# Kernel optimization log

Hardware: AMD Instinct MI355X
Metric: run time of the kernel (lower is better)

The kernel has to match this reference:

```python
import jax, jax.numpy as jnp
import numpy as np

B, S, H, T, N = 32, 512, 1024, 8, 16


def setup_inputs() -> dict:
    key = jax.random.key(0)
    ks = jax.random.split(key, 16)
    sc = 1.0 / np.sqrt(H)
    f32 = jnp.float32
    return {
        "hidden": jax.random.normal(ks[0], (S, B, H), f32),
        "num_encoder_outputs": jax.random.normal(ks[1], (B, N, H), f32),
        "problem_q": jax.random.normal(ks[2], (B, H), f32),
        # GenerateXQs K/V projections
        "Wk": jax.random.normal(ks[3], (H, H), f32) * sc,
        "bk": jax.random.normal(ks[4], (H,), f32) * sc,
        "Wv": jax.random.normal(ks[5], (H, H), f32) * sc,
        "bv": jax.random.normal(ks[6], (H,), f32) * sc,
        # XToQ K/V projections
        "Wk2": jax.random.normal(ks[7], (H, H), f32) * sc,
        "bk2": jax.random.normal(ks[8], (H,), f32) * sc,
        "Wv2": jax.random.normal(ks[9], (H, H), f32) * sc,
        "bv2": jax.random.normal(ks[10], (H,), f32) * sc,
        # XToQ single-layer LSTM (PyTorch gate order i,f,g,o)
        "W_ih": jax.random.normal(ks[11], (4 * H, H), f32) * sc,
        "W_hh": jax.random.normal(ks[12], (4 * H, H), f32) * sc,
        "b_ih": jax.random.normal(ks[13], (4 * H,), f32) * sc,
        "b_hh": jax.random.normal(ks[14], (4 * H,), f32) * sc,
        "num_xs": T,  # all batch items generate T tokens (required for torch.stack)
    }


def _attend(x_bh, keys_bsh, values_bsh):
    # softmax(x @ K^T) @ V, batched over b
    scores = jnp.einsum("bh,bsh->bs", x_bh, keys_bsh)
    attn = jax.nn.softmax(scores, axis=-1)
    return jnp.einsum("bs,bsh->bh", attn, values_bsh)


def reference(hidden, num_encoder_outputs, problem_q,
              Wk, bk, Wv, bv, Wk2, bk2, Wv2, bv2,
              W_ih, W_hh, b_ih, b_hh, num_xs):
    Tn = int(num_xs)
    hidden2 = jnp.swapaxes(hidden, 0, 1)           # [B,S,H]
    keys = hidden2 @ Wk.T + bk                      # [B,S,H]
    values = hidden2 @ Wv.T + bv                    # [B,S,H]

    def gen_step(x, _):
        xn = _attend(x, keys, values)
        return xn, xn

    if Tn > 1:
        _, rest = jax.lax.scan(gen_step, problem_q, None, length=Tn - 1)  # [T-1,B,H]
        final_xs = jnp.concatenate(
            [problem_q[:, None, :], jnp.swapaxes(rest, 0, 1)], axis=1)    # [B,T,H]
    else:
        final_xs = problem_q[:, None, :]

    # XToQ: parallel attention of each generated x over the (projected) hidden
    keys2 = hidden2 @ Wk2.T + bk2
    values2 = hidden2 @ Wv2.T + bv2
    scores = jnp.einsum("bth,bsh->bts", final_xs, keys2)
    attn = jax.nn.softmax(scores, axis=-1)
    qs = jnp.einsum("bts,bsh->bth", attn, values2)  # [B,T,H]

    if Tn > 1:
        # single-layer LSTM over time (PyTorch gate order: i, f, g, o)
        def lstm_step(carry, x_t):
            h, c = carry
            gates = x_t @ W_ih.T + b_ih + h @ W_hh.T + b_hh  # [B,4H]
            i, f, g, o = jnp.split(gates, 4, axis=-1)
            i, f, o = jax.nn.sigmoid(i), jax.nn.sigmoid(f), jax.nn.sigmoid(o)
            g = jnp.tanh(g)
            c = f * c + i * g
            h = o * jnp.tanh(c)
            return (h, c), h

        h0 = jnp.zeros((qs.shape[0], H), qs.dtype)
        c0 = jnp.zeros((qs.shape[0], H), qs.dtype)
        _, outs = jax.lax.scan(lstm_step, (h0, c0), jnp.swapaxes(qs, 0, 1))  # [T,B,H]
        # original appends out1[0] (the t=0 LSTM output) as an extra token
        final_qs = jnp.concatenate([qs, outs[0][:, None, :]], axis=1)        # [B,T+1,H]
    else:
        final_qs = qs

    updated_hidden = jnp.swapaxes(jnp.concatenate([hidden2, final_xs], axis=1), 0, 1)  # [S+T,B,H]
    updated_nums = jnp.concatenate([num_encoder_outputs, final_xs], axis=1)             # [B,N+T,H]
    return (final_qs, updated_hidden, updated_nums)
```

## Files before the change

kernel.cpp:

```cpp
#include <hip/hip_runtime.h>
#include <math.h>

#define Bn 32
#define Sn 512
#define Hn 1024
#define Tn 8
#define Nn 16
#define Gn 4096

__device__ __forceinline__ float wsum(float v){
#pragma unroll
  for (int off = 32; off; off >>= 1) v += __shfl_xor(v, off);
  return v;
}

__device__ __forceinline__ float dot16(float4 a0, float4 a1, float4 a2, float4 a3,
                                       float4 v0, float4 v1, float4 v2, float4 v3){
  float d = a0.x*v0.x + a0.y*v0.y + a0.z*v0.z + a0.w*v0.w;
  d += a1.x*v1.x + a1.y*v1.y + a1.z*v1.z + a1.w*v1.w;
  d += a2.x*v2.x + a2.y*v2.y + a2.z*v2.z + a2.w*v2.w;
  d += a3.x*v3.x + a3.y*v3.y + a3.z*v3.z + a3.w*v3.w;
  return d;
}


__global__ __launch_bounds__(256) void transpose2(
    const float* __restrict__ Wk, const float* __restrict__ Wk2,
    float* __restrict__ WkT, float* __restrict__ Wk2T){
  __shared__ float tile[32][33];
  const float* in  = blockIdx.z ? Wk2  : Wk;
  float*       outp= blockIdx.z ? Wk2T : WkT;
  int tx = threadIdx.x & 31, ty = threadIdx.x >> 5;
  int c0 = blockIdx.x * 32, r0 = blockIdx.y * 32;
#pragma unroll
  for (int k = 0; k < 4; ++k)
    tile[ty + 8*k][tx] = in[(size_t)(r0 + ty + 8*k) * Hn + c0 + tx];
  __syncthreads();
#pragma unroll
  for (int k = 0; k < 4; ++k)
    outp[(size_t)(c0 + ty + 8*k) * Hn + r0 + tx] = tile[tx][ty + 8*k];
}

__global__ __launch_bounds__(256) void prep(
    const float4* __restrict__ nums, const float4* __restrict__ pq,
    float4* __restrict__ un, float4* __restrict__ xs){
  int n = blockIdx.x, b = blockIdx.y;
  if (n < Nn) un[((size_t)b*(Nn+Tn) + n)*256 + threadIdx.x] = nums[((size_t)b*Nn + n)*256 + threadIdx.x];
  else        xs[((size_t)b*Tn)*256 + threadIdx.x] = pq[(size_t)b*256 + threadIdx.x];
}

__global__ __launch_bounds__(256) void finalize_xs(const float4* __restrict__ xs, float4* __restrict__ uh, float4* __restrict__ un){
  int t = blockIdx.x, b = blockIdx.y;
  float4 v = xs[((size_t)b*Tn + t)*256 + threadIdx.x];
  uh[(((size_t)(Sn + t))*Bn + b)*256 + threadIdx.x] = v;
  un[((size_t)b*(Nn+Tn) + Nn + t)*256 + threadIdx.x] = v;
}

template<int FIRST>
__global__ __launch_bounds__(512, 8) void attend8(
    const float* __restrict__ hidden, const float* __restrict__ xk,
    float* __restrict__ ctxp, float* __restrict__ mlp, float* __restrict__ uh)
{
  const int b = blockIdx.y, p = blockIdx.x;
  const int tid = threadIdx.x, lane = tid & 63, w = tid >> 6;
  __shared__ float sM[8], sL[8];
  __shared__ float sacc[8*1024];

  const float4* xp = (const float4*)(xk + (size_t)b*Hn) + lane;
  float4 q0 = xp[0], q1 = xp[64], q2 = xp[128], q3 = xp[192];

  const int s0 = p*16 + w*2;
  size_t r0 = ((size_t)(s0+0)*Bn + b)*Hn, r1 = ((size_t)(s0+1)*Bn + b)*Hn;
  const float4* rp0 = (const float4*)(hidden + r0) + lane;
  const float4* rp1 = (const float4*)(hidden + r1) + lane;
  float4 u0=rp0[0], u1=rp0[64], u2=rp0[128], u3=rp0[192];
  float4 v0=rp1[0], v1=rp1[64], v2=rp1[128], v3=rp1[192];
  if (FIRST){
    float4* w0p = (float4*)(uh + r0) + lane;
    float4* w1p = (float4*)(uh + r1) + lane;
    w0p[0]=u0; w0p[64]=u1; w0p[128]=u2; w0p[192]=u3;
    w1p[0]=v0; w1p[64]=v1; w1p[128]=v2; w1p[192]=v3;
  }
  float d0 = dot16(q0,q1,q2,q3, u0,u1,u2,u3);
  float d1 = dot16(q0,q1,q2,q3, v0,v1,v2,v3);
#pragma unroll
  for (int off = 32; off; off >>= 1){ d0 += __shfl_xor(d0, off); d1 += __shfl_xor(d1, off); }
  float m_run = fmaxf(d0, d1);
  float w0 = __expf(d0 - m_run), w1 = __expf(d1 - m_run);
  float l_run = w0 + w1;
  float4 a0 = make_float4(w0*u0.x + w1*v0.x, w0*u0.y + w1*v0.y, w0*u0.z + w1*v0.z, w0*u0.w + w1*v0.w);
  float4 a1 = make_float4(w0*u1.x + w1*v1.x, w0*u1.y + w1*v1.y, w0*u1.z + w1*v1.z, w0*u1.w + w1*v1.w);
  float4 a2 = make_float4(w0*u2.x + w1*v2.x, w0*u2.y + w1*v2.y, w0*u2.z + w1*v2.z, w0*u2.w + w1*v2.w);
  float4 a3 = make_float4(w0*u3.x + w1*v3.x, w0*u3.y + w1*v3.y, w0*u3.z + w1*v3.z, w0*u3.w + w1*v3.w);

  {
    int sl0 = (lane*4 + 0) ^ (lane & 7);
    int sl1 = (lane*4 + 1) ^ (lane & 7);
    int sl2 = (lane*4 + 2) ^ (lane & 7);
    int sl3 = (lane*4 + 3) ^ (lane & 7);
    *(float4*)(sacc + w*1024 + sl0*4) = a0;
    *(float4*)(sacc + w*1024 + sl1*4) = a1;
    *(float4*)(sacc + w*1024 + sl2*4) = a2;
    *(float4*)(sacc + w*1024 + sl3*4) = a3;
  }
  if (lane == 0){ sM[w] = m_run; sL[w] = l_run; }
  __syncthreads();
  float M = sM[0];
#pragma unroll
  for (int i = 1; i < 8; ++i) M = fmaxf(M, sM[i]);
  float wex[8];
#pragma unroll
  for (int i = 0; i < 8; ++i) wex[i] = __expf(sM[i] - M);
#pragma unroll
  for (int h0 = 0; h0 < 1024; h0 += 512){
    int c = h0 + tid;
    int k = c >> 8, l = (c >> 2) & 63, j = c & 3;
    int fo = ((((l << 2) + k) ^ (l & 7)) << 2) + j;
    float s = 0.f;
#pragma unroll
    for (int i = 0; i < 8; ++i) s = fmaf(sacc[i*1024 + fo], wex[i], s);
    ctxp[((size_t)b*32 + p)*1024 + c] = s;
  }
  if (tid == 0){
    float L = 0.f;
#pragma unroll
    for (int i = 0; i < 8; ++i) L = fmaf(sL[i], wex[i], L);
    mlp[((size_t)b*32 + p)*2]     = M;
    mlp[((size_t)b*32 + p)*2 + 1] = L;
  }
}

__global__ __launch_bounds__(256) void mv1(
    const float* __restrict__ X, int xstride,
    const float* __restrict__ M, float* __restrict__ part,
    int nj, int ktiles)
{
  __shared__ float wt[64*128];
  __shared__ float xl[64*32];
  const int t  = threadIdx.x;
  const int j0 = blockIdx.x * 128;
  const int kb = blockIdx.y;
  const int r0 = blockIdx.z * 32;
  const int R  = gridDim.z * 32;
  const int tj = t & 31, tr = t >> 5;
  float acc[4][4] = {{0.f,0.f,0.f,0.f},{0.f,0.f,0.f,0.f},{0.f,0.f,0.f,0.f},{0.f,0.f,0.f,0.f}};

  for (int kt = 0; kt < ktiles; ++kt){
    const int k0 = (kb*ktiles + kt)*64;
    __syncthreads();
    {
      int j = t >> 1;
      int kqb = (t & 1) * 8;
      const float* Mrow = M + (size_t)(j0 + j)*1024 + k0;
#pragma unroll
      for (int c = 0; c < 8; ++c){
        float4 v = *(const float4*)(Mrow + (kqb + c)*4);
        int kk = (kqb + c)*4;
        wt[(kk+0)*128 + j] = v.x;
        wt[(kk+1)*128 + j] = v.y;
        wt[(kk+2)*128 + j] = v.z;
        wt[(kk+3)*128 + j] = v.w;
      }
      int r = t >> 3;
      int kq0 = t & 7;
#pragma unroll
      for (int c = 0; c < 2; ++c){
        int kk = (kq0 + c*8)*4;
        float4 v = *(const float4*)(X + (size_t)(r0 + r)*xstride + k0 + kk);
        xl[(kk+0)*32 + r] = v.x;
        xl[(kk+1)*32 + r] = v.y;
        xl[(kk+2)*32 + r] = v.z;
        xl[(kk+3)*32 + r] = v.w;
      }
    }
    __syncthreads();
#pragma unroll 4
    for (int k = 0; k < 64; ++k){
      float4 w4 = *(const float4*)(wt + k*128 + tj*4);
      float4 x4 = *(const float4*)(xl + k*32  + tr*4);
      acc[0][0] = fmaf(x4.x, w4.x, acc[0][0]);
      acc[0][1] = fmaf(x4.x, w4.y, acc[0][1]);
      acc[0][2] = fmaf(x4.x, w4.z, acc[0][2]);
      acc[0][3] = fmaf(x4.x, w4.w, acc[0][3]);
      acc[1][0] = fmaf(x4.y, w4.x, acc[1][0]);
      acc[1][1] = fmaf(x4.y, w4.y, acc[1][1]);
      acc[1][2] = fmaf(x4.y, w4.z, acc[1][2]);
      acc[1][3] = fmaf(x4.y, w4.w, acc[1][3]);
      acc[2][0] = fmaf(x4.z, w4.x, acc[2][0]);
      acc[2][1] = fmaf(x4.z, w4.y, acc[2][1]);
      acc[2][2] = fmaf(x4.z, w4.z, acc[2][2]);
      acc[2][3] = fmaf(x4.z, w4.w, acc[2][3]);
      acc[3][0] = fmaf(x4.w, w4.x, acc[3][0]);
      acc[3][1] = fmaf(x4.w, w4.y, acc[3][1]);
      acc[3][2] = fmaf(x4.w, w4.z, acc[3][2]);
      acc[3][3] = fmaf(x4.w, w4.w, acc[3][3]);
    }
  }
  const size_t base = ((size_t)kb*R + r0 + tr*4)*nj + j0 + tj*4;
#pragma unroll
  for (int i = 0; i < 4; ++i)
    *(float4*)(part + base + (size_t)i*nj) = make_float4(acc[i][0], acc[i][1], acc[i][2], acc[i][3]);
}

__global__ __launch_bounds__(256) void mv2(
    const float* __restrict__ part, int R, int njshift, int KB,
    const float* __restrict__ b1, const float* __restrict__ b2,
    float* __restrict__ out, int rpgshift, int opg)
{
  int idx = blockIdx.x*256 + threadIdx.x;
  int nj = 1 << njshift;
  int r = idx >> njshift, j = idx & (nj - 1);
  float s = 0.f;
  if (b1) s += b1[j];
  if (b2) s += b2[j];
  size_t stride = (size_t)R << njshift;
  for (int kb = 0; kb < KB; ++kb) s += part[(size_t)kb*stride + idx];
  int orow = ((r >> rpgshift) * opg) + (r & ((1 << rpgshift) - 1));
  out[((size_t)orow << njshift) + j] = s;
}

__global__ __launch_bounds__(256) void genstep(
    const float* __restrict__ ctxp, const float* __restrict__ mlp,
    const float* __restrict__ Wv, float* __restrict__ part)
{
  __shared__ float wt[64*128];
  __shared__ float xl[64*32];
  const int t  = threadIdx.x;
  const int j0 = blockIdx.x * 128;
  const int kb = blockIdx.y;
  const int k0 = kb*64;
  const int tj = t & 31, tr = t >> 5;

  {
    int j = t >> 1;
    int kqb = (t & 1) * 8;
    const float* Mrow = Wv + (size_t)(j0 + j)*1024 + k0;
#pragma unroll
    for (int c = 0; c < 8; ++c){
      float4 v = *(const float4*)(Mrow + (kqb + c)*4);
      int kk = (kqb + c)*4;
      wt[(kk+0)*128 + j] = v.x;
      wt[(kk+1)*128 + j] = v.y;
      wt[(kk+2)*128 + j] = v.z;
      wt[(kk+3)*128 + j] = v.w;
    }
  }
  {
    int b = t >> 3, kk = (t & 7)*8;
    float mx = -1e30f;
#pragma unroll
    for (int i = 0; i < 32; ++i) mx = fmaxf(mx, mlp[((size_t)b*32 + i)*2]);
    float L = 0.f;
    float a8[8] = {0.f,0.f,0.f,0.f,0.f,0.f,0.f,0.f};
#pragma unroll 4
    for (int i = 0; i < 32; ++i){
      float m = mlp[((size_t)b*32 + i)*2];
      float l = mlp[((size_t)b*32 + i)*2 + 1];
      float we = __expf(m - mx);
      L = fmaf(l, we, L);
      const float* cp = ctxp + ((size_t)b*32 + i)*1024 + k0 + kk;
      float4 u0 = *(const float4*)cp;
      float4 u1 = *(const float4*)(cp + 4);
      a8[0] = fmaf(we, u0.x, a8[0]); a8[1] = fmaf(we, u0.y, a8[1]);
      a8[2] = fmaf(we, u0.z, a8[2]); a8[3] = fmaf(we, u0.w, a8[3]);
      a8[4] = fmaf(we, u1.x, a8[4]); a8[5] = fmaf(we, u1.y, a8[5]);
      a8[6] = fmaf(we, u1.z, a8[6]); a8[7] = fmaf(we, u1.w, a8[7]);
    }
    float inv = 1.f / L;
#pragma unroll
    for (int q = 0; q < 8; ++q) xl[(kk + q)*32 + b] = a8[q]*inv;
  }
  __syncthreads();
  float acc[4][4] = {{0.f,0.f,0.f,0.f},{0.f,0.f,0.f,0.f},{0.f,0.f,0.f,0.f},{0.f,0.f,0.f,0.f}};
#pragma unroll 4
  for (int k = 0; k < 64; ++k){
    float4 w4 = *(const float4*)(wt + k*128 + tj*4);
    float4 x4 = *(const float4*)(xl + k*32  + tr*4);
    acc[0][0] = fmaf(x4.x, w4.x, acc[0][0]);
    acc[0][1] = fmaf(x4.x, w4.y, acc[0][1]);
    acc[0][2] = fmaf(x4.x, w4.z, acc[0][2]);
    acc[0][3] = fmaf(x4.x, w4.w, acc[0][3]);
    acc[1][0] = fmaf(x4.y, w4.x, acc[1][0]);
    acc[1][1] = fmaf(x4.y, w4.y, acc[1][1]);
    acc[1][2] = fmaf(x4.y, w4.z, acc[1][2]);
    acc[1][3] = fmaf(x4.y, w4.w, acc[1][3]);
    acc[2][0] = fmaf(x4.z, w4.x, acc[2][0]);
    acc[2][1] = fmaf(x4.z, w4.y, acc[2][1]);
    acc[2][2] = fmaf(x4.z, w4.z, acc[2][2]);
    acc[2][3] = fmaf(x4.z, w4.w, acc[2][3]);
    acc[3][0] = fmaf(x4.w, w4.x, acc[3][0]);
    acc[3][1] = fmaf(x4.w, w4.y, acc[3][1]);
    acc[3][2] = fmaf(x4.w, w4.z, acc[3][2]);
    acc[3][3] = fmaf(x4.w, w4.w, acc[3][3]);
  }
  const size_t base = ((size_t)kb*32 + tr*4)*1024 + j0 + tj*4;
#pragma unroll
  for (int i = 0; i < 4; ++i)
    *(float4*)(part + base + (size_t)i*1024) = make_float4(acc[i][0], acc[i][1], acc[i][2], acc[i][3]);
}


__global__ __launch_bounds__(512) void scores2_kernel(
    const float* __restrict__ hidden, const float* __restrict__ xk2, float* __restrict__ sc)
{
  int b = blockIdx.y, p = blockIdx.x;
  int lane = threadIdx.x & 63, w = threadIdx.x >> 6;
  int t0 = (w & 3) * 2, rh = w >> 2;
  const float4* qa = (const float4*)(xk2 + ((size_t)b*Tn + t0  )*Hn) + lane;
  const float4* qb = (const float4*)(xk2 + ((size_t)b*Tn + t0+1)*Hn) + lane;
  float4 a0=qa[0], a1=qa[64], a2=qa[128], a3=qa[192];
  float4 c0=qb[0], c1=qb[64], c2=qb[128], c3=qb[192];
#pragma unroll 2
  for (int r = 0; r < 8; ++r){
    int s = p*16 + rh*8 + r;
    const float4* row = (const float4*)(hidden + ((size_t)s*Bn + b)*Hn) + lane;
    float4 v0=row[0], v1=row[64], v2=row[128], v3=row[192];
    float d0 = wsum(dot16(a0,a1,a2,a3, v0,v1,v2,v3));
    float d1 = wsum(dot16(c0,c1,c2,c3, v0,v1,v2,v3));
    if (lane == 0){
      sc[((size_t)b*Tn + t0  )*Sn + s] = d0;
      sc[((size_t)b*Tn + t0+1)*Sn + s] = d1;
    }
  }
}

__global__ __launch_bounds__(512) void ctx2f(
    const float* __restrict__ hidden, const float* __restrict__ scraw, float* __restrict__ ctx2)
{
  int b = blockIdx.y, hc = blockIdx.x, tid = threadIdx.x;
  __shared__ float al[Tn*Sn];
  for (int i = tid; i < Tn*Sn; i += 512) al[i] = scraw[(size_t)b*Tn*Sn + i];
  __syncthreads();
  {
    int r = tid >> 6, lane = tid & 63;
    float mx = -1e30f;
#pragma unroll
    for (int k = 0; k < 8; ++k) mx = fmaxf(mx, al[r*Sn + lane + k*64]);
#pragma unroll
    for (int off = 32; off; off >>= 1) mx = fmaxf(mx, __shfl_xor(mx, off));
    float e[8], s = 0.f;
#pragma unroll
    for (int k = 0; k < 8; ++k){ e[k] = __expf(al[r*Sn + lane + k*64] - mx); s += e[k]; }
#pragma unroll
    for (int off = 32; off; off >>= 1) s += __shfl_xor(s, off);
    float inv = 1.f / s;
#pragma unroll
    for (int k = 0; k < 8; ++k) al[r*Sn + lane + k*64] = e[k] * inv;
  }
  __syncthreads();
  int hloc = tid & 127, tg = tid >> 7;
  int h = hc*128 + hloc;
  int t0 = tg*2;
  float acc0 = 0.f, acc1 = 0.f;
#pragma unroll 4
  for (int s = 0; s < Sn; ++s){
    float v = hidden[((size_t)s*Bn + b)*Hn + h];
    acc0 = fmaf(al[t0*Sn + s],     v, acc0);
    acc1 = fmaf(al[(t0+1)*Sn + s], v, acc1);
  }
  ctx2[((size_t)b*Tn + t0  )*Hn + h] = acc0;
  ctx2[((size_t)b*Tn + t0+1)*Hn + h] = acc1;
}

__global__ __launch_bounds__(256) void lstm_fused(
    const float* __restrict__ part, const float* __restrict__ b_ih,
    const float* __restrict__ b_hh, float* __restrict__ fq)
{
  int idx = blockIdx.x*256 + threadIdx.x;
  int b = idx >> 10, h = idx & 1023;
  const size_t stride = (size_t)32*Gn;
  float gi = b_ih[h] + b_hh[h];
  float gg = b_ih[2048+h] + b_hh[2048+h];
  float go = b_ih[3072+h] + b_hh[3072+h];
  for (int kb = 0; kb < 16; ++kb){
    const float* pp = part + (size_t)kb*stride + (size_t)b*Gn;
    gi += pp[h]; gg += pp[2048+h]; go += pp[3072+h];
  }
  float si = 1.f/(1.f + __expf(-gi));
  float so = 1.f/(1.f + __expf(-go));
  float c  = si * tanhf(gg);
  fq[((size_t)b*(Tn+1) + Tn)*Hn + h] = so * tanhf(c);
}


extern "C" void kernel_launch(void* const* d_in, const int* in_sizes, int n_in,
                              void* d_out, int out_size, void* d_ws, size_t ws_size,
                              hipStream_t stream) {
  const float* hidden = (const float*)d_in[0];
  const float* nums   = (const float*)d_in[1];
  const float* pq     = (const float*)d_in[2];
  const float* Wk     = (const float*)d_in[3];
  const float* Wv     = (const float*)d_in[5];
  const float* bv     = (const float*)d_in[6];
  const float* Wk2    = (const float*)d_in[7];
  const float* Wv2    = (const float*)d_in[9];
  const float* bv2    = (const float*)d_in[10];
  const float* W_ih   = (const float*)d_in[11];
  const float* b_ih   = (const float*)d_in[13];
  const float* b_hh   = (const float*)d_in[14];

  float* out = (float*)d_out;
  float* fq  = out;
  float* uh  = out + (size_t)Bn*(Tn+1)*Hn;
  float* un  = uh + (size_t)(Sn+Tn)*Bn*Hn;

  float* ws    = (float*)d_ws;
  float* xs    = ws;
  float* ctxp  = ws + 262144;
  float* mlp   = ws + 1310720;
  float* xk    = ws + 1312768;
  float* xk2   = ws + 1345536;
  float* sc2   = ws + 1607680;
  float* ctx2v = ws + 1738752;
  float* partX = ws + 2000896;
  float* partK = ws + 2525184;
  float* WkT   = ws + 3049472;
  float* Wk2T  = ws + 4098048;
  float* partS = partX;
  float* partL = WkT;

  transpose2<<<dim3(32,32,2), 256, 0, stream>>>(Wk, Wk2, WkT, Wk2T);
  prep<<<dim3(Nn+1, Bn), 256, 0, stream>>>((const float4*)nums, (const float4*)pq, (float4*)un, (float4*)xs);

  mv1<<<dim3(8,16,1), 256, 0, stream>>>(pq, Hn, WkT, partK, Hn, 1);
  mv2<<<128, 256, 0, stream>>>(partK, 32, 10, 16, nullptr, nullptr, xk, 0, 1);

  for (int t = 1; t < Tn; ++t){
    if (t == 1) attend8<1><<<dim3(32,Bn), 512, 0, stream>>>(hidden, xk, ctxp, mlp, uh);
    else        attend8<0><<<dim3(32,Bn), 512, 0, stream>>>(hidden, xk, ctxp, mlp, uh);
    genstep<<<dim3(8,16), 256, 0, stream>>>(ctxp, mlp, Wv, partX);
    mv2<<<128, 256, 0, stream>>>(partX, 32, 10, 16, bv, nullptr, xs + (size_t)t*Hn, 0, Tn);
    if (t < Tn-1){
      mv1<<<dim3(8,16,1), 256, 0, stream>>>(xs + (size_t)t*Hn, Tn*Hn, WkT, partK, Hn, 1);
      mv2<<<128, 256, 0, stream>>>(partK, 32, 10, 16, nullptr, nullptr, xk, 0, 1);
    }
  }

  mv1<<<dim3(8,4,8), 256, 0, stream>>>(xs, Hn, Wk2T, partS, Hn, 4);
  mv2<<<1024, 256, 0, stream>>>(partS, 256, 10, 4, nullptr, nullptr, xk2, 0, 1);
  scores2_kernel<<<dim3(32, Bn), 512, 0, stream>>>(hidden, xk2, sc2);
  ctx2f<<<dim3(8, Bn), 512, 0, stream>>>(hidden, sc2, ctx2v);
  mv1<<<dim3(8,4,8), 256, 0, stream>>>(ctx2v, Hn, Wv2, partS, Hn, 4);
  mv2<<<1024, 256, 0, stream>>>(partS, 256, 10, 4, bv2, nullptr, fq, 3, Tn+1);

  mv1<<<dim3(32,16,1), 256, 0, stream>>>(fq, (Tn+1)*Hn, W_ih, partL, Gn, 1);
  lstm_fused<<<128, 256, 0, stream>>>(partL, b_ih, b_hh, fq);

  finalize_xs<<<dim3(Tn, Bn), 256, 0, stream>>>((const float4*)xs, (float4*)uh, (float4*)un);
}
```

Baseline: 418.3 us.

## Widen attention blocks to 32 rows and split ctx2 over sequence chunks

The per-step attention kernel now has each warp handle 4 sequence rows (32 per block), halving the grid and the number of partial contexts that genstep must merge. It computes a block-wide max before exponentiation, so the partials are combined without rescaling. The second-stage context kernel is split into a standalone softmax, a sequence-chunked partial accumulation across 4x more blocks, and a reduction kernel. The goal is more parallelism in ctx2 and fewer partials in the serial loop, at the cost of extra launches, higher register pressure and fewer blocks in attend.

```diff
diff --git a/kernel.cpp b/kernel.cpp
--- a/kernel.cpp
+++ b/kernel.cpp
@@ -57,7 +57,7 @@
 }
 
 template<int FIRST>
-__global__ __launch_bounds__(512, 8) void attend8(
+__global__ __launch_bounds__(512, 4) void attend9(
     const float* __restrict__ hidden, const float* __restrict__ xk,
     float* __restrict__ ctxp, float* __restrict__ mlp, float* __restrict__ uh)
 {
@@ -69,29 +69,56 @@
   const float4* xp = (const float4*)(xk + (size_t)b*Hn) + lane;
   float4 q0 = xp[0], q1 = xp[64], q2 = xp[128], q3 = xp[192];
 
-  const int s0 = p*16 + w*2;
-  size_t r0 = ((size_t)(s0+0)*Bn + b)*Hn, r1 = ((size_t)(s0+1)*Bn + b)*Hn;
-  const float4* rp0 = (const float4*)(hidden + r0) + lane;
-  const float4* rp1 = (const float4*)(hidden + r1) + lane;
-  float4 u0=rp0[0], u1=rp0[64], u2=rp0[128], u3=rp0[192];
-  float4 v0=rp1[0], v1=rp1[64], v2=rp1[128], v3=rp1[192];
+  const int s0 = p*32 + w*4;
+  size_t ro[4];
+#pragma unroll
+  for (int i = 0; i < 4; ++i) ro[i] = ((size_t)(s0+i)*Bn + b)*Hn;
+  float4 u[4][4];
+#pragma unroll
+  for (int i = 0; i < 4; ++i){
+    const float4* rp = (const float4*)(hidden + ro[i]) + lane;
+    u[i][0]=rp[0]; u[i][1]=rp[64]; u[i][2]=rp[128]; u[i][3]=rp[192];
+  }
   if (FIRST){
-    float4* w0p = (float4*)(uh + r0) + lane;
-    float4* w1p = (float4*)(uh + r1) + lane;
-    w0p[0]=u0; w0p[64]=u1; w0p[128]=u2; w0p[192]=u3;
-    w1p[0]=v0; w1p[64]=v1; w1p[128]=v2; w1p[192]=v3;
-  }
-  float d0 = dot16(q0,q1,q2,q3, u0,u1,u2,u3);
-  float d1 = dot16(q0,q1,q2,q3, v0,v1,v2,v3);
-#pragma unroll
-  for (int off = 32; off; off >>= 1){ d0 += __shfl_xor(d0, off); d1 += __shfl_xor(d1, off); }
-  float m_run = fmaxf(d0, d1);
-  float w0 = __expf(d0 - m_run), w1 = __expf(d1 - m_run);
-  float l_run = w0 + w1;
-  float4 a0 = make_float4(w0*u0.x + w1*v0.x, w0*u0.y + w1*v0.y, w0*u0.z + w1*v0.z, w0*u0.w + w1*v0.w);
-  float4 a1 = make_float4(w0*u1.x + w1*v1.x, w0*u1.y + w1*v1.y, w0*u1.z + w1*v1.z, w0*u1.w + w1*v1.w);
-  float4 a2 = make_float4(w0*u2.x + w1*v2.x, w0*u2.y + w1*v2.y, w0*u2.z + w1*v2.z, w0*u2.w + w1*v2.w);
-  float4 a3 = make_float4(w0*u3.x + w1*v3.x, w0*u3.y + w1*v3.y, w0*u3.z + w1*v3.z, w0*u3.w + w1*v3.w);
+#pragma unroll
+    for (int i = 0; i < 4; ++i){
+      float4* wp = (float4*)(uh + ro[i]) + lane;
+      wp[0]=u[i][0]; wp[64]=u[i][1]; wp[128]=u[i][2]; wp[192]=u[i][3];
+    }
+  }
+  float d[4];
+#pragma unroll
+  for (int i = 0; i < 4; ++i) d[i] = dot16(q0,q1,q2,q3, u[i][0],u[i][1],u[i][2],u[i][3]);
+#pragma unroll
+  for (int off = 32; off; off >>= 1){
+#pragma unroll
+    for (int i = 0; i < 4; ++i) d[i] += __shfl_xor(d[i], off);
+  }
+  float mw = fmaxf(fmaxf(d[0], d[1]), fmaxf(d[2], d[3]));
+  sM[w] = mw;
+  __syncthreads();
+  float M = sM[0];
+#pragma unroll
+  for (int i = 1; i < 8; ++i) M = fmaxf(M, sM[i]);
+  float wi[4], lw = 0.f;
+#pragma unroll
+  for (int i = 0; i < 4; ++i){ wi[i] = __expf(d[i] - M); lw += wi[i]; }
+  float4 a0, a1, a2, a3;
+  a0 = make_float4(wi[0]*u[0][0].x, wi[0]*u[0][0].y, wi[0]*u[0][0].z, wi[0]*u[0][0].w);
+  a1 = make_float4(wi[0]*u[0][1].x, wi[0]*u[0][1].y, wi[0]*u[0][1].z, wi[0]*u[0][1].w);
+  a2 = make_float4(wi[0]*u[0][2].x, wi[0]*u[0][2].y, wi[0]*u[0][2].z, wi[0]*u[0][2].w);
+  a3 = make_float4(wi[0]*u[0][3].x, wi[0]*u[0][3].y, wi[0]*u[0][3].z, wi[0]*u[0][3].w);
+#pragma unroll
+  for (int i = 1; i < 4; ++i){
+    a0.x = fmaf(wi[i], u[i][0].x, a0.x); a0.y = fmaf(wi[i], u[i][0].y, a0.y);
+    a0.z = fmaf(wi[i], u[i][0].z, a0.z); a0.w = fmaf(wi[i], u[i][0].w, a0.w);
+    a1.x = fmaf(wi[i], u[i][1].x, a1.x); a1.y = fmaf(wi[i], u[i][1].y, a1.y);
+    a1.z = fmaf(wi[i], u[i][1].z, a1.z); a1.w = fmaf(wi[i], u[i][1].w, a1.w);
+    a2.x = fmaf(wi[i], u[i][2].x, a2.x); a2.y = fmaf(wi[i], u[i][2].y, a2.y);
+    a2.z = fmaf(wi[i], u[i][2].z, a2.z); a2.w = fmaf(wi[i], u[i][2].w, a2.w);
+    a3.x = fmaf(wi[i], u[i][3].x, a3.x); a3.y = fmaf(wi[i], u[i][3].y, a3.y);
+    a3.z = fmaf(wi[i], u[i][3].z, a3.z); a3.w = fmaf(wi[i], u[i][3].w, a3.w);
+  }
 
   {
     int sl0 = (lane*4 + 0) ^ (lane & 7);
@@ -103,14 +130,8 @@
     *(float4*)(sacc + w*1024 + sl2*4) = a2;
     *(float4*)(sacc + w*1024 + sl3*4) = a3;
   }
-  if (lane == 0){ sM[w] = m_run; sL[w] = l_run; }
-  __syncthreads();
-  float M = sM[0];
-#pragma unroll
-  for (int i = 1; i < 8; ++i) M = fmaxf(M, sM[i]);
-  float wex[8];
-#pragma unroll
-  for (int i = 0; i < 8; ++i) wex[i] = __expf(sM[i] - M);
+  if (lane == 0) sL[w] = lw;
+  __syncthreads();
 #pragma unroll
   for (int h0 = 0; h0 < 1024; h0 += 512){
     int c = h0 + tid;
@@ -118,15 +139,15 @@
     int fo = ((((l << 2) + k) ^ (l & 7)) << 2) + j;
     float s = 0.f;
 #pragma unroll
-    for (int i = 0; i < 8; ++i) s = fmaf(sacc[i*1024 + fo], wex[i], s);
-    ctxp[((size_t)b*32 + p)*1024 + c] = s;
+    for (int i = 0; i < 8; ++i) s += sacc[i*1024 + fo];
+    ctxp[((size_t)b*16 + p)*1024 + c] = s;
   }
   if (tid == 0){
     float L = 0.f;
 #pragma unroll
-    for (int i = 0; i < 8; ++i) L = fmaf(sL[i], wex[i], L);
-    mlp[((size_t)b*32 + p)*2]     = M;
-    mlp[((size_t)b*32 + p)*2 + 1] = L;
+    for (int i = 0; i < 8; ++i) L += sL[i];
+    mlp[((size_t)b*16 + p)*2]     = M;
+    mlp[((size_t)b*16 + p)*2 + 1] = L;
   }
 }
 
@@ -249,16 +270,16 @@
     int b = t >> 3, kk = (t & 7)*8;
     float mx = -1e30f;
 #pragma unroll
-    for (int i = 0; i < 32; ++i) mx = fmaxf(mx, mlp[((size_t)b*32 + i)*2]);
+    for (int i = 0; i < 16; ++i) mx = fmaxf(mx, mlp[((size_t)b*16 + i)*2]);
     float L = 0.f;
     float a8[8] = {0.f,0.f,0.f,0.f,0.f,0.f,0.f,0.f};
 #pragma unroll 4
-    for (int i = 0; i < 32; ++i){
-      float m = mlp[((size_t)b*32 + i)*2];
-      float l = mlp[((size_t)b*32 + i)*2 + 1];
+    for (int i = 0; i < 16; ++i){
+      float m = mlp[((size_t)b*16 + i)*2];
+      float l = mlp[((size_t)b*16 + i)*2 + 1];
       float we = __expf(m - mx);
       L = fmaf(l, we, L);
-      const float* cp = ctxp + ((size_t)b*32 + i)*1024 + k0 + kk;
+      const float* cp = ctxp + ((size_t)b*16 + i)*1024 + k0 + kk;
       float4 u0 = *(const float4*)cp;
       float4 u1 = *(const float4*)(cp + 4);
       a8[0] = fmaf(we, u0.x, a8[0]); a8[1] = fmaf(we, u0.y, a8[1]);
@@ -324,42 +345,57 @@
   }
 }
 
-__global__ __launch_bounds__(512) void ctx2f(
-    const float* __restrict__ hidden, const float* __restrict__ scraw, float* __restrict__ ctx2)
-{
-  int b = blockIdx.y, hc = blockIdx.x, tid = threadIdx.x;
-  __shared__ float al[Tn*Sn];
-  for (int i = tid; i < Tn*Sn; i += 512) al[i] = scraw[(size_t)b*Tn*Sn + i];
-  __syncthreads();
-  {
-    int r = tid >> 6, lane = tid & 63;
-    float mx = -1e30f;
-#pragma unroll
-    for (int k = 0; k < 8; ++k) mx = fmaxf(mx, al[r*Sn + lane + k*64]);
-#pragma unroll
-    for (int off = 32; off; off >>= 1) mx = fmaxf(mx, __shfl_xor(mx, off));
-    float e[8], s = 0.f;
-#pragma unroll
-    for (int k = 0; k < 8; ++k){ e[k] = __expf(al[r*Sn + lane + k*64] - mx); s += e[k]; }
-#pragma unroll
-    for (int off = 32; off; off >>= 1) s += __shfl_xor(s, off);
-    float inv = 1.f / s;
-#pragma unroll
-    for (int k = 0; k < 8; ++k) al[r*Sn + lane + k*64] = e[k] * inv;
-  }
-  __syncthreads();
-  int hloc = tid & 127, tg = tid >> 7;
-  int h = hc*128 + hloc;
-  int t0 = tg*2;
+__global__ __launch_bounds__(512) void softmax512(float* __restrict__ sc){
+  int row = blockIdx.x, tid = threadIdx.x, lane = tid & 63, w = tid >> 6;
+  float v = sc[(size_t)row*Sn + tid];
+  float mx = v;
+#pragma unroll
+  for (int off = 32; off; off >>= 1) mx = fmaxf(mx, __shfl_xor(mx, off));
+  __shared__ float sm[8], ss[8];
+  if (lane == 0) sm[w] = mx;
+  __syncthreads();
+  mx = sm[0];
+#pragma unroll
+  for (int i = 1; i < 8; ++i) mx = fmaxf(mx, sm[i]);
+  float e = __expf(v - mx);
+  float s = e;
+#pragma unroll
+  for (int off = 32; off; off >>= 1) s += __shfl_xor(s, off);
+  if (lane == 0) ss[w] = s;
+  __syncthreads();
+  float tot = 0.f;
+#pragma unroll
+  for (int i = 0; i < 8; ++i) tot += ss[i];
+  sc[(size_t)row*Sn + tid] = e / tot;
+}
+
+__global__ __launch_bounds__(512) void ctx2p(
+    const float* __restrict__ hidden, const float* __restrict__ attn, float* __restrict__ part)
+{
+  int hc = blockIdx.x, sc = blockIdx.y, b = blockIdx.z;
+  int tid = threadIdx.x, hloc = tid & 127, tg = tid >> 7;
+  __shared__ float al[Tn*128];
+  for (int idx = tid; idx < Tn*128; idx += 512){
+    int t = idx >> 7, si = idx & 127;
+    al[idx] = attn[((size_t)b*Tn + t)*Sn + sc*128 + si];
+  }
+  __syncthreads();
+  int h = hc*128 + hloc, t0 = tg*2;
   float acc0 = 0.f, acc1 = 0.f;
 #pragma unroll 4
-  for (int s = 0; s < Sn; ++s){
+  for (int si = 0; si < 128; ++si){
+    int s = sc*128 + si;
     float v = hidden[((size_t)s*Bn + b)*Hn + h];
-    acc0 = fmaf(al[t0*Sn + s],     v, acc0);
-    acc1 = fmaf(al[(t0+1)*Sn + s], v, acc1);
-  }
-  ctx2[((size_t)b*Tn + t0  )*Hn + h] = acc0;
-  ctx2[((size_t)b*Tn + t0+1)*Hn + h] = acc1;
+    acc0 = fmaf(al[t0*128 + si],     v, acc0);
+    acc1 = fmaf(al[(t0+1)*128 + si], v, acc1);
+  }
+  part[(((size_t)sc*Bn + b)*Tn + t0  )*Hn + h] = acc0;
+  part[(((size_t)sc*Bn + b)*Tn + t0+1)*Hn + h] = acc1;
+}
+
+__global__ __launch_bounds__(256) void ctx2r(const float* __restrict__ part, float* __restrict__ out){
+  int idx = blockIdx.x*256 + threadIdx.x;
+  out[idx] = part[idx] + part[262144 + idx] + part[524288 + idx] + part[786432 + idx];
 }
 
 __global__ __launch_bounds__(256) void lstm_fused(
@@ -417,6 +453,7 @@
   float* WkT   = ws + 3049472;
   float* Wk2T  = ws + 4098048;
   float* partS = partX;
+  float* c2part= partX;
   float* partL = WkT;
 
   transpose2<<<dim3(32,32,2), 256, 0, stream>>>(Wk, Wk2, WkT, Wk2T);
@@ -426,8 +463,8 @@
   mv2<<<128, 256, 0, stream>>>(partK, 32, 10, 16, nullptr, nullptr, xk, 0, 1);
 
   for (int t = 1; t < Tn; ++t){
-    if (t == 1) attend8<1><<<dim3(32,Bn), 512, 0, stream>>>(hidden, xk, ctxp, mlp, uh);
-    else        attend8<0><<<dim3(32,Bn), 512, 0, stream>>>(hidden, xk, ctxp, mlp, uh);
+    if (t == 1) attend9<1><<<dim3(16,Bn), 512, 0, stream>>>(hidden, xk, ctxp, mlp, uh);
+    else        attend9<0><<<dim3(16,Bn), 512, 0, stream>>>(hidden, xk, ctxp, mlp, uh);
     genstep<<<dim3(8,16), 256, 0, stream>>>(ctxp, mlp, Wv, partX);
     mv2<<<128, 256, 0, stream>>>(partX, 32, 10, 16, bv, nullptr, xs + (size_t)t*Hn, 0, Tn);
     if (t < Tn-1){
@@ -439,7 +476,9 @@
   mv1<<<dim3(8,4,8), 256, 0, stream>>>(xs, Hn, Wk2T, partS, Hn, 4);
   mv2<<<1024, 256, 0, stream>>>(partS, 256, 10, 4, nullptr, nullptr, xk2, 0, 1);
   scores2_kernel<<<dim3(32, Bn), 512, 0, stream>>>(hidden, xk2, sc2);
-  ctx2f<<<dim3(8, Bn), 512, 0, stream>>>(hidden, sc2, ctx2v);
+  softmax512<<<Bn*Tn, 512, 0, stream>>>(sc2);
+  ctx2p<<<dim3(8, 4, Bn), 512, 0, stream>>>(hidden, sc2, c2part);
+  ctx2r<<<1024, 256, 0, stream>>>(c2part, ctx2v);
   mv1<<<dim3(8,4,8), 256, 0, stream>>>(ctx2v, Hn, Wv2, partS, Hn, 4);
   mv2<<<1024, 256, 0, stream>>>(partS, 256, 10, 4, bv2, nullptr, fq, 3, Tn+1);
 
```

Result: faster. 379.7 us (-9.2%).
